# Optimization experiments

Hardware: AMD Instinct MI355X
Metric: run time of the kernel (lower is better)

Reference implementation:

```python
import jax, jax.numpy as jnp
import numpy as np

NT, NC = 100000, 25000
ETT, ECT = 800000, 400000
DIN_T, DIN_C = 64, 32
H, C = 4, 32
HID = H * C  # 128
SLOPE = 0.2  # GATConv LeakyReLU negative slope


def setup_inputs() -> dict:
    key = jax.random.key(0)
    ks = jax.random.split(key, 24)
    def p(i, shape, s=0.05):
        return jax.random.normal(ks[i], shape, dtype=jnp.float32) * s
    return {
        'x_target': jax.random.normal(ks[0], (NT, DIN_T), dtype=jnp.float32),
        'x_context': jax.random.normal(ks[1], (NC, DIN_C), dtype=jnp.float32),
        'edge_tt': jax.random.randint(ks[2], (2, ETT), 0, NT),
        'edge_ct_src': jax.random.randint(ks[3], (ECT,), 0, NC),
        'edge_ct_dst': jax.random.randint(ks[4], (ECT,), 0, NT),
        'W_pre_t': p(5, (DIN_T, HID)), 'b_pre_t': jnp.zeros((HID,), jnp.float32),
        'W_pre_c': p(6, (DIN_C, HID)), 'b_pre_c': jnp.zeros((HID,), jnp.float32),
        'W_sd': p(7, (HID, HID)), 'att_src_sd': p(8, (H, C)), 'att_dst_sd': p(9, (H, C)), 'b_sd': jnp.zeros((HID,), jnp.float32),
        'W_ds': p(10, (HID, HID)), 'att_src_ds': p(11, (H, C)), 'att_dst_ds': p(12, (H, C)), 'b_ds': jnp.zeros((HID,), jnp.float32),
        'W_ct_src': p(13, (HID, HID)), 'W_ct_dst': p(14, (HID, HID)), 'att_src_ct': p(15, (H, C)), 'att_dst_ct': p(16, (H, C)), 'b_ct': jnp.zeros((HID,), jnp.float32),
        'W_out': p(17, (HID, HID)), 'b_out': jnp.zeros((HID,), jnp.float32),
    }


def _gat(h_src, h_dst, att_s, att_d, src, dst, n_dst, bias):
    # h_src: [N_src,H,C] transformed src feats; h_dst: [N_dst,H,C]
    a_s = jnp.einsum('nhc,hc->nh', h_src, att_s)  # [N_src,H]
    a_d = jnp.einsum('nhc,hc->nh', h_dst, att_d)  # [N_dst,H]
    e = a_s[src] + a_d[dst]                        # [E,H]
    e = jnp.where(e > 0, e, SLOPE * e)             # LeakyReLU(0.2)
    m = jax.ops.segment_max(e, dst, num_segments=n_dst)  # stable softmax per dst
    ex = jnp.exp(e - m[dst])
    den = jax.ops.segment_sum(ex, dst, num_segments=n_dst)
    alpha = ex / den[dst]                          # [E,H]
    msg = h_src[src] * alpha[:, :, None]           # [E,H,C]
    out = jax.ops.segment_sum(msg, dst, num_segments=n_dst)
    return out.reshape(n_dst, H * C) + bias


def reference(x_target, x_context, edge_tt, edge_ct_src, edge_ct_dst,
              W_pre_t, b_pre_t, W_pre_c, b_pre_c,
              W_sd, att_src_sd, att_dst_sd, b_sd,
              W_ds, att_src_ds, att_dst_ds, b_ds,
              W_ct_src, W_ct_dst, att_src_ct, att_dst_ct, b_ct,
              W_out, b_out):
    # HeteroDictLinear pretransform + relu
    h_t = jax.nn.relu(x_target @ W_pre_t + b_pre_t)   # [NT,128]
    h_c = jax.nn.relu(x_context @ W_pre_c + b_pre_c)  # [NC,128]
    res = h_t
    # DirGATConv on (target,to,target): forward + reversed, each w/ self-loops
    loops = jnp.arange(NT)
    src_f = jnp.concatenate([edge_tt[0], loops]); dst_f = jnp.concatenate([edge_tt[1], loops])
    src_r = jnp.concatenate([edge_tt[1], loops]); dst_r = jnp.concatenate([edge_tt[0], loops])
    hs = (h_t @ W_sd).reshape(NT, H, C)
    out_sd = _gat(hs, hs, att_src_sd, att_dst_sd, src_f, dst_f, NT, b_sd)
    hd = (h_t @ W_ds).reshape(NT, H, C)
    out_ds = _gat(hd, hd, att_src_ds, att_dst_ds, src_r, dst_r, NT, b_ds)
    out_tt = 0.5 * out_sd + 0.5 * out_ds  # (1-alpha), alpha with alpha=0.5
    # bipartite GATConv on (context,to,target), no self loops
    hcs = (h_c @ W_ct_src).reshape(NC, H, C)
    htd = (h_t @ W_ct_dst).reshape(NT, H, C)
    out_ct = _gat(hcs, htd, att_src_ct, att_dst_ct, edge_ct_src, edge_ct_dst, NT, b_ct)
    # HeteroConv aggr='mean' over the two edge types hitting 'target'
    x = 0.5 * (out_tt + out_ct)
    x = jax.nn.relu(x + res)  # skip connection + relu
    return x @ W_out + b_out
```

## Files before the change

kernel.cpp:

```cpp
#include <hip/hip_runtime.h>
#include <cstdint>
#include <cstddef>

typedef unsigned short u16;
typedef unsigned int u32;

#define NT 100000
#define NC 25000
#define ETT 800000
#define ECT 400000
#define SLOPE 0.2f
#define OFFS (NT + 4)

#define NBK 782
#define NBLK 256
#define CHT ((ETT + NBLK - 1) / NBLK)
#define CHC ((ECT + NBLK - 1) / NBLK)
#define TOTC (3 * NBK * NBLK)
#define NSB ((TOTC + 2047) / 2048)

typedef __attribute__((ext_vector_type(8))) short bf16x8;
typedef __attribute__((ext_vector_type(4))) float f32x4;

__device__ __forceinline__ u16 f2bf(float f) {
  u32 u = __float_as_uint(f);
  u32 r = (u >> 16) & 1u;
  return (u16)((u + 0x7fffu + r) >> 16);
}
__device__ __forceinline__ float lof(u32 p) { return __uint_as_float(p << 16); }
__device__ __forceinline__ float hif(u32 p) { return __uint_as_float(p & 0xffff0000u); }

__global__ __launch_bounds__(256) void pre_t_kernel(const float* __restrict__ in,
    const float* __restrict__ W, const float* __restrict__ bias,
    const float* __restrict__ fold_cd, u16* __restrict__ h_t,
    float* __restrict__ aD, int N)
{
  __shared__ float s_in[32][33];
  __shared__ float s_W[32][128];
  __shared__ float s_fold[512];
  const int t = threadIdx.x;
  s_fold[t] = fold_cd[t];
  s_fold[t + 256] = fold_cd[t + 256];
  const int row0 = blockIdx.x * 32;
  const int rl = t >> 3, cg = t & 7;
  const int gr = row0 + rl;
  float acc[4][4];
  for (int g = 0; g < 4; ++g)
    for (int j = 0; j < 4; ++j)
      acc[g][j] = bias[g * 32 + cg * 4 + j];
  for (int kc = 0; kc < 64; kc += 32) {
    {
      float4 f = make_float4(0.f, 0.f, 0.f, 0.f);
      if (gr < N) f = *(const float4*)(in + (size_t)gr * 64 + kc + cg * 4);
      s_in[rl][cg * 4 + 0] = f.x; s_in[rl][cg * 4 + 1] = f.y;
      s_in[rl][cg * 4 + 2] = f.z; s_in[rl][cg * 4 + 3] = f.w;
    }
    for (int j = 0; j < 4; ++j) {
      const int idx = t + j * 256;
      const int k = idx >> 5, c4 = (idx & 31) * 4;
      *(float4*)&s_W[k][c4] = *(const float4*)(W + (size_t)(kc + k) * 128 + c4);
    }
    __syncthreads();
#pragma unroll 8
    for (int k = 0; k < 32; ++k) {
      const float a = s_in[rl][k];
      for (int g = 0; g < 4; ++g) {
        const float4 w = *(const float4*)&s_W[k][g * 32 + cg * 4];
        acc[g][0] = fmaf(a, w.x, acc[g][0]);
        acc[g][1] = fmaf(a, w.y, acc[g][1]);
        acc[g][2] = fmaf(a, w.z, acc[g][2]);
        acc[g][3] = fmaf(a, w.w, acc[g][3]);
      }
    }
    __syncthreads();
  }
  if (gr < N) {
    float p0 = 0.f, p1 = 0.f, p2 = 0.f, p3 = 0.f;
    for (int g = 0; g < 4; ++g) {
      for (int j = 0; j < 4; ++j) acc[g][j] = fmaxf(acc[g][j], 0.f);
      uint2 pk;
      pk.x = (u32)f2bf(acc[g][0]) | ((u32)f2bf(acc[g][1]) << 16);
      pk.y = (u32)f2bf(acc[g][2]) | ((u32)f2bf(acc[g][3]) << 16);
      *(uint2*)(h_t + (size_t)gr * 128 + g * 32 + cg * 4) = pk;
      for (int j = 0; j < 4; ++j) {
        const int col = g * 32 + cg * 4 + j;
        const float4 f4 = *(const float4*)&s_fold[col * 4];
        const float a = acc[g][j];
        p0 = fmaf(a, f4.x, p0); p1 = fmaf(a, f4.y, p1);
        p2 = fmaf(a, f4.z, p2); p3 = fmaf(a, f4.w, p3);
      }
    }
    for (int m = 1; m < 8; m <<= 1) {
      p0 += __shfl_xor(p0, m); p1 += __shfl_xor(p1, m);
      p2 += __shfl_xor(p2, m); p3 += __shfl_xor(p3, m);
    }
    if (cg == 0) *(float4*)(aD + (size_t)gr * 4) = make_float4(p0, p1, p2, p3);
  }
}

__global__ __launch_bounds__(256) void prep_kernel(
    const float* __restrict__ Wsd, const float* __restrict__ AsSd, const float* __restrict__ AdSd,
    const float* __restrict__ Wds, const float* __restrict__ AsDs, const float* __restrict__ AdDs,
    const float* __restrict__ Wout, u16* __restrict__ bf_sd, u16* __restrict__ bf_ds,
    u16* __restrict__ bf_out,
    const float* __restrict__ Wcd, const float* __restrict__ attD,
    const float* __restrict__ bsd, const float* __restrict__ bds, const float* __restrict__ bct,
    float* __restrict__ fold_cd, float* __restrict__ cbias)
{
  const int b = blockIdx.x;
  const int tid = threadIdx.x;
  if (b == 3) {
    if (tid < 128) {
      for (int h = 0; h < 4; ++h) {
        float s = 0.f;
        for (int c = 0; c < 32; ++c)
          s = fmaf(Wcd[tid * 128 + h * 32 + c], attD[h * 32 + c], s);
        fold_cd[tid * 4 + h] = s;
      }
      cbias[tid] = 0.25f * bsd[tid] + 0.25f * bds[tid] + 0.5f * bct[tid];
    }
    return;
  }
  __shared__ float fS[512], fD[512];
  const float* W = (b == 0) ? Wsd : (b == 1) ? Wds : Wout;
  const float* As = (b == 0) ? AsSd : AsDs;
  const float* Ad = (b == 0) ? AdSd : AdDs;
  u16* out = (b == 0) ? bf_sd : (b == 1) ? bf_ds : bf_out;
  const int tiles = (b == 2) ? 8 : 9;
  if (b < 2) {
    if (tid < 128) {
      for (int h = 0; h < 4; ++h) {
        float s1 = 0.f, s2 = 0.f;
        for (int c = 0; c < 32; ++c) {
          const float wv = W[tid * 128 + h * 32 + c];
          s1 = fmaf(wv, As[h * 32 + c], s1);
          s2 = fmaf(wv, Ad[h * 32 + c], s2);
        }
        fS[tid * 4 + h] = s1; fD[tid * 4 + h] = s2;
      }
    }
    __syncthreads();
  }
  const int total = tiles * 4 * 64 * 8;
  for (int i = tid; i < total; i += 256) {
    const int j = i & 7, lane = (i >> 3) & 63, ks = (i >> 9) & 3, t = i >> 11;
    const int k = ks * 32 + (lane >> 4) * 8 + j;
    const int n = t * 16 + (lane & 15);
    float v;
    if (n < 128) v = W[k * 128 + n];
    else if (n < 132) v = fS[k * 4 + (n - 128)];
    else if (n < 136) v = fD[k * 4 + (n - 132)];
    else v = 0.f;
    out[i] = f2bf(v);
  }
}

__global__ __launch_bounds__(256) void mfma_logits2_kernel(
    const short* __restrict__ A, const short* __restrict__ Bsd, const short* __restrict__ Bds,
    u16* __restrict__ hs, float* __restrict__ aSsd, float* __restrict__ aDsd,
    u16* __restrict__ hd, float* __restrict__ aSds, float* __restrict__ aDds, int M)
{
  __shared__ __align__(16) float lds[4][16][148];
  const int wv = threadIdx.x >> 6, lane = threadIdx.x & 63;
  const int quad = lane >> 4, l16 = lane & 15;
  const int row0 = blockIdx.x * 64 + wv * 16;
  const int arow = min(row0 + l16, M - 1);
  const short* ap = A + (size_t)arow * 128 + quad * 8;
  bf16x8 af[4];
  for (int ks = 0; ks < 4; ++ks) af[ks] = *(const bf16x8*)(ap + ks * 32);
  const int row = row0 + l16;
  const int idx = lane & 7, rr = lane >> 3;
  for (int pass = 0; pass < 2; ++pass) {
    const short* B = pass ? Bds : Bsd;
    u16* outb = pass ? hd : hs;
    float* aS = pass ? aSds : aSsd;
    float* aD = pass ? aDds : aDsd;
    f32x4 acc[9];
    for (int t = 0; t < 9; ++t) acc[t] = (f32x4){0.f, 0.f, 0.f, 0.f};
    for (int ks = 0; ks < 4; ++ks)
      for (int t = 0; t < 9; ++t) {
        const bf16x8 bf = *(const bf16x8*)(B + ((t * 4 + ks) * 64 + lane) * 8);
        acc[t] = __builtin_amdgcn_mfma_f32_16x16x32_bf16(af[ks], bf, acc[t], 0, 0, 0);
      }
    for (int t = 0; t < 9; ++t)
      for (int r = 0; r < 4; ++r)
        lds[wv][quad * 4 + r][t * 16 + l16] = acc[t][r];
    __syncthreads();
    if (row < M) {
      for (int g = 0; g < 8; ++g) {
        const f32x4 v = *(const f32x4*)&lds[wv][l16][g * 16 + quad * 4];
        uint2 pk;
        pk.x = (u32)f2bf(v[0]) | ((u32)f2bf(v[1]) << 16);
        pk.y = (u32)f2bf(v[2]) | ((u32)f2bf(v[3]) << 16);
        *(uint2*)(outb + (size_t)row * 128 + g * 16 + quad * 4) = pk;
      }
    }
    for (int p = 0; p < 2; ++p) {
      const int lr = p * 8 + rr;
      const int n = row0 + lr;
      if (n < M) {
        const float v = lds[wv][lr][128 + idx];
        if (idx < 4) aS[(size_t)n * 4 + idx] = v;
        else aD[(size_t)n * 4 + idx - 4] = v;
      }
    }
    __syncthreads();
  }
}

__global__ __launch_bounds__(256) void mfma_out_kernel(
    const short* __restrict__ A, const short* __restrict__ B,
    const float* __restrict__ bias, float* __restrict__ out, int M)
{
  __shared__ __align__(16) float lds[4][16][132];
  const int wv = threadIdx.x >> 6, lane = threadIdx.x & 63;
  const int quad = lane >> 4, l16 = lane & 15;
  const int row0 = blockIdx.x * 64 + wv * 16;
  const int arow = min(row0 + l16, M - 1);
  const short* ap = A + (size_t)arow * 128 + quad * 8;
  bf16x8 af[4];
  for (int ks = 0; ks < 4; ++ks) af[ks] = *(const bf16x8*)(ap + ks * 32);
  f32x4 acc[8];
  for (int t = 0; t < 8; ++t) acc[t] = (f32x4){0.f, 0.f, 0.f, 0.f};
  for (int ks = 0; ks < 4; ++ks)
    for (int t = 0; t < 8; ++t) {
      const bf16x8 bf = *(const bf16x8*)(B + ((t * 4 + ks) * 64 + lane) * 8);
      acc[t] = __builtin_amdgcn_mfma_f32_16x16x32_bf16(af[ks], bf, acc[t], 0, 0, 0);
    }
  for (int t = 0; t < 8; ++t)
    for (int r = 0; r < 4; ++r)
      lds[wv][quad * 4 + r][t * 16 + l16] = acc[t][r];
  __syncthreads();
  const int row = row0 + l16;
  if (row < M) {
    for (int g = 0; g < 8; ++g) {
      const int col = g * 16 + quad * 4;
      f32x4 v = *(const f32x4*)&lds[wv][l16][col];
      const f32x4 b4 = *(const f32x4*)(bias + col);
      v = v + b4;
      *(f32x4*)(out + (size_t)row * 128 + col) = v;
    }
  }
}

__global__ __launch_bounds__(256) void ctx_kernel(const float* __restrict__ x_c,
    const float* __restrict__ Wpc, const float* __restrict__ bpc,
    const float* __restrict__ Wcs, const float* __restrict__ attS,
    u16* __restrict__ hc_bf, float* __restrict__ aS, int N)
{
  __shared__ float s_in[32][33];
  __shared__ float s_W[32][128];
  __shared__ float s_h[32][132];
  const int t = threadIdx.x;
  const int row0 = blockIdx.x * 32;
  const int rl = t >> 3, cg = t & 7;
  const int gr = row0 + rl;
  {
    float4 f = make_float4(0.f, 0.f, 0.f, 0.f);
    if (gr < N) f = *(const float4*)(x_c + (size_t)gr * 32 + cg * 4);
    s_in[rl][cg * 4 + 0] = f.x; s_in[rl][cg * 4 + 1] = f.y;
    s_in[rl][cg * 4 + 2] = f.z; s_in[rl][cg * 4 + 3] = f.w;
  }
  for (int j = 0; j < 4; ++j) {
    const int idx = t + j * 256;
    const int k = idx >> 5, c4 = (idx & 31) * 4;
    *(float4*)&s_W[k][c4] = *(const float4*)(Wpc + (size_t)k * 128 + c4);
  }
  __syncthreads();
  float acc[4][4];
  for (int g = 0; g < 4; ++g)
    for (int j = 0; j < 4; ++j) acc[g][j] = bpc[g * 32 + cg * 4 + j];
#pragma unroll 8
  for (int k = 0; k < 32; ++k) {
    const float a = s_in[rl][k];
    for (int g = 0; g < 4; ++g) {
      const float4 w = *(const float4*)&s_W[k][g * 32 + cg * 4];
      acc[g][0] = fmaf(a, w.x, acc[g][0]);
      acc[g][1] = fmaf(a, w.y, acc[g][1]);
      acc[g][2] = fmaf(a, w.z, acc[g][2]);
      acc[g][3] = fmaf(a, w.w, acc[g][3]);
    }
  }
  for (int g = 0; g < 4; ++g)
    *(float4*)&s_h[rl][g * 32 + cg * 4] =
        make_float4(fmaxf(acc[g][0], 0.f), fmaxf(acc[g][1], 0.f),
                    fmaxf(acc[g][2], 0.f), fmaxf(acc[g][3], 0.f));
  __syncthreads();
  float acc2[4][4];
  for (int g = 0; g < 4; ++g)
    for (int j = 0; j < 4; ++j) acc2[g][j] = 0.f;
  for (int kc = 0; kc < 128; kc += 32) {
    for (int j = 0; j < 4; ++j) {
      const int idx = t + j * 256;
      const int k = idx >> 5, c4 = (idx & 31) * 4;
      *(float4*)&s_W[k][c4] = *(const float4*)(Wcs + (size_t)(kc + k) * 128 + c4);
    }
    __syncthreads();
#pragma unroll 8
    for (int k = 0; k < 32; ++k) {
      const float a = s_h[rl][kc + k];
      for (int g = 0; g < 4; ++g) {
        const float4 w = *(const float4*)&s_W[k][g * 32 + cg * 4];
        acc2[g][0] = fmaf(a, w.x, acc2[g][0]);
        acc2[g][1] = fmaf(a, w.y, acc2[g][1]);
        acc2[g][2] = fmaf(a, w.z, acc2[g][2]);
        acc2[g][3] = fmaf(a, w.w, acc2[g][3]);
      }
    }
    __syncthreads();
  }
  if (gr < N) {
    float pS[4];
    for (int g = 0; g < 4; ++g) {
      uint2 pk;
      pk.x = (u32)f2bf(acc2[g][0]) | ((u32)f2bf(acc2[g][1]) << 16);
      pk.y = (u32)f2bf(acc2[g][2]) | ((u32)f2bf(acc2[g][3]) << 16);
      *(uint2*)(hc_bf + (size_t)gr * 128 + g * 32 + cg * 4) = pk;
      const float4 as4 = *(const float4*)(attS + g * 32 + cg * 4);
      pS[g] = acc2[g][0] * as4.x + acc2[g][1] * as4.y + acc2[g][2] * as4.z + acc2[g][3] * as4.w;
    }
    for (int m = 1; m < 8; m <<= 1)
      for (int g = 0; g < 4; ++g) pS[g] += __shfl_xor(pS[g], m);
    if (cg == 0)
      *(float4*)(aS + (size_t)gr * 4) = make_float4(pS[0], pS[1], pS[2], pS[3]);
  }
}

__global__ __launch_bounds__(256) void hist_blk_kernel(const int* __restrict__ tt_src,
    const int* __restrict__ tt_dst, const int* __restrict__ ect_d, int* __restrict__ cntblk)
{
  __shared__ int h[3 * NBK];
  const int t = threadIdx.x, b = blockIdx.x;
  for (int i = t; i < 3 * NBK; i += 256) h[i] = 0;
  __syncthreads();
  const int lo = b * CHT, hi = min(lo + CHT, ETT);
  for (int i = lo + t; i < hi; i += 256) {
    atomicAdd(&h[tt_dst[i] >> 7], 1);
    atomicAdd(&h[NBK + (tt_src[i] >> 7)], 1);
  }
  const int lo2 = b * CHC, hi2 = min(lo2 + CHC, ECT);
  for (int i = lo2 + t; i < hi2; i += 256)
    atomicAdd(&h[2 * NBK + (ect_d[i] >> 7)], 1);
  __syncthreads();
  for (int i = t; i < 3 * NBK; i += 256)
    cntblk[(size_t)i * NBLK + b] = h[i];
}

__global__ __launch_bounds__(256) void scan2_blk_kernel(const int* __restrict__ in,
    int* __restrict__ out, int* __restrict__ bsum)
{
  const int t = threadIdx.x, b = blockIdx.x;
  const int idx = b * 2048 + t * 8;
  int v[8];
  int s = 0;
  if (idx < TOTC) {
    const int4 q0 = *(const int4*)(in + idx);
    const int4 q1 = *(const int4*)(in + idx + 4);
    int x;
    x = q0.x; v[0] = s; s += x;  x = q0.y; v[1] = s; s += x;
    x = q0.z; v[2] = s; s += x;  x = q0.w; v[3] = s; s += x;
    x = q1.x; v[4] = s; s += x;  x = q1.y; v[5] = s; s += x;
    x = q1.z; v[6] = s; s += x;  x = q1.w; v[7] = s; s += x;
  } else {
    for (int j = 0; j < 8; ++j) v[j] = 0;
  }
  __shared__ int sh[256];
  sh[t] = s;
  __syncthreads();
  for (int d = 1; d < 256; d <<= 1) {
    const int u = (t >= d) ? sh[t - d] : 0;
    __syncthreads();
    sh[t] += u;
    __syncthreads();
  }
  const int excl = (t == 0) ? 0 : sh[t - 1];
  if (idx < TOTC) {
    int4 q0, q1;
    q0.x = excl + v[0]; q0.y = excl + v[1]; q0.z = excl + v[2]; q0.w = excl + v[3];
    q1.x = excl + v[4]; q1.y = excl + v[5]; q1.z = excl + v[6]; q1.w = excl + v[7];
    *(int4*)(out + idx) = q0;
    *(int4*)(out + idx + 4) = q1;
  }
  if (t == 255) bsum[b] = sh[255];
}

__global__ __launch_bounds__(512) void scan2_top_kernel(const int* __restrict__ bsum,
    int* __restrict__ bpre)
{
  __shared__ int sh[512];
  const int t = threadIdx.x;
  const int orig = (t < NSB) ? bsum[t] : 0;
  sh[t] = orig;
  __syncthreads();
  for (int d = 1; d < 512; d <<= 1) {
    const int v = (t >= d) ? sh[t - d] : 0;
    __syncthreads();
    sh[t] += v;
    __syncthreads();
  }
  if (t < NSB) bpre[t] = sh[t] - orig;
}

__global__ __launch_bounds__(256) void scan2_add_kernel(const int* __restrict__ bpre,
    int* __restrict__ out)
{
  const int t = threadIdx.x, b = blockIdx.x;
  const int bp = bpre[b];
  const int idx = b * 2048 + t * 8;
  if (idx < TOTC) {
    int4 q0 = *(const int4*)(out + idx);
    int4 q1 = *(const int4*)(out + idx + 4);
    q0.x += bp; q0.y += bp; q0.z += bp; q0.w += bp;
    q1.x += bp; q1.y += bp; q1.z += bp; q1.w += bp;
    *(int4*)(out + idx) = q0;
    *(int4*)(out + idx + 4) = q1;
  }
}

__global__ __launch_bounds__(256) void bin_kernel(const int* __restrict__ tt_src,
    const int* __restrict__ tt_dst, const int* __restrict__ ect_s, const int* __restrict__ ect_d,
    const int* __restrict__ scanned, u32* __restrict__ bin)
{
  __shared__ int cur[3 * NBK];
  const int t = threadIdx.x, b = blockIdx.x;
  for (int i = t; i < 3 * NBK; i += 256)
    cur[i] = scanned[(size_t)i * NBLK + b];
  __syncthreads();
  const int lo = b * CHT, hi = min(lo + CHT, ETT);
  for (int i = lo + t; i < hi; i += 256) {
    const int s = tt_src[i], d = tt_dst[i];
    int p = atomicAdd(&cur[d >> 7], 1);
    bin[p] = ((u32)(d & 127) << 17) | (u32)s;
    p = atomicAdd(&cur[NBK + (s >> 7)], 1);
    bin[p] = ((u32)(s & 127) << 17) | (u32)d;
  }
  const int lo2 = b * CHC, hi2 = min(lo2 + CHC, ECT);
  for (int i = lo2 + t; i < hi2; i += 256) {
    const int s = ect_s[i], d = ect_d[i];
    const int p = atomicAdd(&cur[2 * NBK + (d >> 7)], 1);
    bin[p] = ((u32)(d & 127) << 17) | (u32)s;
  }
}

__global__ __launch_bounds__(256) void bucket_fill_kernel(const int* __restrict__ scanned,
    const u32* __restrict__ bin, int* __restrict__ offs, int* __restrict__ big_el)
{
  const int rel = blockIdx.x / NBK;
  const int bucket = blockIdx.x - rel * NBK;
  const int t = threadIdx.x;
  __shared__ int s_cnt[128], s_exc[128], s_cur[128];
  if (t < 128) s_cnt[t] = 0;
  __syncthreads();
  const int base = scanned[(size_t)blockIdx.x * NBLK];
  const int nxt = (blockIdx.x == 3 * NBK - 1) ? (2 * ETT + ECT)
                                              : scanned[((size_t)blockIdx.x + 1) * NBLK];
  const int size = nxt - base;
  for (int i = t; i < size; i += 256)
    atomicAdd(&s_cnt[bin[base + i] >> 17], 1);
  __syncthreads();
  if (t < 128) s_exc[t] = s_cnt[t];
  __syncthreads();
  for (int d = 1; d < 128; d <<= 1) {
    int v = 0;
    if (t < 128 && t >= d) v = s_exc[t - d];
    __syncthreads();
    if (t < 128) s_exc[t] += v;
    __syncthreads();
  }
  const int relbase = rel * ETT;
  const int obase = base - relbase;
  int* off_rel = offs + (size_t)rel * OFFS;
  const int node0 = bucket * 128;
  if (t < 128) {
    const int excl = s_exc[t] - s_cnt[t];
    s_cur[t] = obase + excl;
    if (node0 + t < NT) off_rel[node0 + t] = obase + excl;
  }
  if (t == 0 && bucket == NBK - 1) off_rel[NT] = obase + size;
  __syncthreads();
  int* el_rel = big_el + relbase;
  for (int i = t; i < size; i += 256) {
    const u32 e = bin[base + i];
    const int pos = atomicAdd(&s_cur[e >> 17], 1);
    el_rel[pos] = (int)(e & 0x1FFFFu);
  }
}

__device__ __forceinline__ void gat_pipe16(const int* __restrict__ off,
    const int* __restrict__ el, const float* __restrict__ aS, const float* __restrict__ aD,
    const u16* __restrict__ hb, int d, int h, int cb, int self_loop, float w,
    float* __restrict__ acc)
{
  const float ad = aD[(size_t)d * 4 + h];
  const int beg = off[d];
  const int m = off[d + 1] - beg;
  const int cnt = m + self_loop;
  if (cnt <= 0) return;
  float den = 0.f;
  float a0 = 0.f, a1 = 0.f, a2 = 0.f, a3 = 0.f, a4 = 0.f, a5 = 0.f, a6 = 0.f, a7 = 0.f;
  int sB = (1 < m) ? el[beg + 1] : d;
  {
    const int sA0 = (0 < m) ? el[beg] : d;
    float eA = aS[(size_t)sA0 * 4 + h];
    uint4 pA = *(const uint4*)(hb + (size_t)sA0 * 128 + cb);
    for (int k = 0; k < cnt; ++k) {
      const int sC = (k + 2 < m) ? el[beg + k + 2] : d;
      const float eB = aS[(size_t)sB * 4 + h];
      const uint4 pB = *(const uint4*)(hb + (size_t)sB * 128 + cb);
      float ea = eA + ad;
      ea = ea > 0.f ? ea : SLOPE * ea;
      const float ex = __expf(ea);
      den += ex;
      a0 = fmaf(ex, lof(pA.x), a0); a1 = fmaf(ex, hif(pA.x), a1);
      a2 = fmaf(ex, lof(pA.y), a2); a3 = fmaf(ex, hif(pA.y), a3);
      a4 = fmaf(ex, lof(pA.z), a4); a5 = fmaf(ex, hif(pA.z), a5);
      a6 = fmaf(ex, lof(pA.w), a6); a7 = fmaf(ex, hif(pA.w), a7);
      eA = eB; pA = pB; sB = sC;
    }
  }
  const float s = w / den;
  acc[0] = fmaf(a0, s, acc[0]); acc[1] = fmaf(a1, s, acc[1]);
  acc[2] = fmaf(a2, s, acc[2]); acc[3] = fmaf(a3, s, acc[3]);
  acc[4] = fmaf(a4, s, acc[4]); acc[5] = fmaf(a5, s, acc[5]);
  acc[6] = fmaf(a6, s, acc[6]); acc[7] = fmaf(a7, s, acc[7]);
}

__global__ __launch_bounds__(256) void gather_all_kernel(
    const int* __restrict__ off_f, const int* __restrict__ el_f,
    const float* __restrict__ aS_sd, const float* __restrict__ aD_sd, const u16* __restrict__ hs,
    const int* __restrict__ off_r, const int* __restrict__ el_r,
    const float* __restrict__ aS_ds, const float* __restrict__ aD_ds, const u16* __restrict__ hd,
    const int* __restrict__ off_c, const int* __restrict__ el_c,
    const float* __restrict__ aS_ct, const float* __restrict__ aD_ct, const u16* __restrict__ hc,
    const u16* __restrict__ skip, const float* __restrict__ cbias, u16* __restrict__ x)
{
  const int d = blockIdx.x * 16 + (threadIdx.x >> 4);
  if (d >= NT) return;
  const int lg = threadIdx.x & 15;
  const int h = lg >> 2;
  const int cb = lg * 8;
  float acc[8];
  for (int i = 0; i < 8; ++i) acc[i] = 0.f;
  gat_pipe16(off_f, el_f, aS_sd, aD_sd, hs, d, h, cb, 1, 0.25f, acc);
  gat_pipe16(off_r, el_r, aS_ds, aD_ds, hd, d, h, cb, 1, 0.25f, acc);
  gat_pipe16(off_c, el_c, aS_ct, aD_ct, hc, d, h, cb, 0, 0.5f, acc);
  const uint4 sk = *(const uint4*)(skip + (size_t)d * 128 + cb);
  const float4 cb0 = *(const float4*)(cbias + cb);
  const float4 cb1 = *(const float4*)(cbias + cb + 4);
  const float o0 = fmaxf(acc[0] + cb0.x + lof(sk.x), 0.f);
  const float o1 = fmaxf(acc[1] + cb0.y + hif(sk.x), 0.f);
  const float o2 = fmaxf(acc[2] + cb0.z + lof(sk.y), 0.f);
  const float o3 = fmaxf(acc[3] + cb0.w + hif(sk.y), 0.f);
  const float o4 = fmaxf(acc[4] + cb1.x + lof(sk.z), 0.f);
  const float o5 = fmaxf(acc[5] + cb1.y + hif(sk.z), 0.f);
  const float o6 = fmaxf(acc[6] + cb1.z + lof(sk.w), 0.f);
  const float o7 = fmaxf(acc[7] + cb1.w + hif(sk.w), 0.f);
  uint4 r;
  r.x = (u32)f2bf(o0) | ((u32)f2bf(o1) << 16);
  r.y = (u32)f2bf(o2) | ((u32)f2bf(o3) << 16);
  r.z = (u32)f2bf(o4) | ((u32)f2bf(o5) << 16);
  r.w = (u32)f2bf(o6) | ((u32)f2bf(o7) << 16);
  *(uint4*)(x + (size_t)d * 128 + cb) = r;
}

extern "C" void kernel_launch(void* const* d_in, const int* in_sizes, int n_in,
                              void* d_out, int out_size, void* d_ws, size_t ws_size,
                              hipStream_t stream)
{
  const float* x_t   = (const float*)d_in[0];
  const float* x_c   = (const float*)d_in[1];
  const int*   e_tt  = (const int*)d_in[2];
  const int*   ect_s = (const int*)d_in[3];
  const int*   ect_d = (const int*)d_in[4];
  const float* Wpt = (const float*)d_in[5];   const float* bpt = (const float*)d_in[6];
  const float* Wpc = (const float*)d_in[7];   const float* bpc = (const float*)d_in[8];
  const float* Wsd = (const float*)d_in[9];   const float* As_sd = (const float*)d_in[10];
  const float* Ad_sd = (const float*)d_in[11]; const float* bsd = (const float*)d_in[12];
  const float* Wds = (const float*)d_in[13];  const float* As_ds = (const float*)d_in[14];
  const float* Ad_ds = (const float*)d_in[15]; const float* bds = (const float*)d_in[16];
  const float* Wcs = (const float*)d_in[17];  const float* Wcd = (const float*)d_in[18];
  const float* As_ct = (const float*)d_in[19]; const float* Ad_ct = (const float*)d_in[20];
  const float* bct = (const float*)d_in[21];
  const float* Wout = (const float*)d_in[22]; const float* bout = (const float*)d_in[23];

  char* p = (char*)d_ws;
  size_t off = 0;
  auto alloc = [&](size_t bytes) { char* r = p + off; off += (bytes + 255) & ~(size_t)255; return r; };
  u16* ht_bf   = (u16*)alloc((size_t)NT * 128 * 2);
  u16* hs_bf   = (u16*)alloc((size_t)NT * 128 * 2);
  u16* hd_bf   = (u16*)alloc((size_t)NT * 128 * 2);
  u16* hc_bf   = (u16*)alloc((size_t)NC * 128 * 2);
  u16* x_bf    = (u16*)alloc((size_t)NT * 128 * 2);
  float* aS_sd = (float*)alloc((size_t)NT * 4 * 4);
  float* aD_sd = (float*)alloc((size_t)NT * 4 * 4);
  float* aS_ds = (float*)alloc((size_t)NT * 4 * 4);
  float* aD_ds = (float*)alloc((size_t)NT * 4 * 4);
  float* aS_ct = (float*)alloc((size_t)NC * 4 * 4);
  float* aD_ct = (float*)alloc((size_t)NT * 4 * 4);
  int* cntblk  = (int*)alloc((size_t)TOTC * 4);
  int* scanned = (int*)alloc((size_t)TOTC * 4);
  u32* bin     = (u32*)alloc((size_t)(2 * ETT + ECT) * 4);
  int* big_el  = (int*)alloc((size_t)(2 * ETT + ECT) * 4);
  int* offs    = (int*)alloc((size_t)3 * OFFS * 4);
  int* bsum    = (int*)alloc((size_t)NSB * 4);
  int* bpre    = (int*)alloc((size_t)NSB * 4);
  float* fold_cd = (float*)alloc(512 * 4);
  float* cbias   = (float*)alloc(128 * 4);
  u16* bfrag_sd  = (u16*)alloc((size_t)9 * 4 * 64 * 8 * 2);
  u16* bfrag_ds  = (u16*)alloc((size_t)9 * 4 * 64 * 8 * 2);
  u16* bfrag_out = (u16*)alloc((size_t)8 * 4 * 64 * 8 * 2);

  int* off_f = offs;
  int* off_r = offs + OFFS;
  int* off_c = offs + 2 * OFFS;
  int* el_f = big_el;
  int* el_r = big_el + ETT;
  int* el_c = big_el + 2 * ETT;

  const int* tt_src = e_tt;
  const int* tt_dst = e_tt + ETT;

  const int gT = (NT + 31) / 32;
  const int gC = (NC + 31) / 32;
  const int gM = (NT + 63) / 64;

  hist_blk_kernel<<<NBLK, 256, 0, stream>>>(tt_src, tt_dst, ect_d, cntblk);
  scan2_blk_kernel<<<NSB, 256, 0, stream>>>(cntblk, scanned, bsum);
  scan2_top_kernel<<<1, 512, 0, stream>>>(bsum, bpre);
  scan2_add_kernel<<<NSB, 256, 0, stream>>>(bpre, scanned);
  bin_kernel<<<NBLK, 256, 0, stream>>>(tt_src, tt_dst, ect_s, ect_d, scanned, bin);
  bucket_fill_kernel<<<3 * NBK, 256, 0, stream>>>(scanned, bin, offs, big_el);

  prep_kernel<<<4, 256, 0, stream>>>(Wsd, As_sd, Ad_sd, Wds, As_ds, Ad_ds, Wout,
                                     bfrag_sd, bfrag_ds, bfrag_out,
                                     Wcd, Ad_ct, bsd, bds, bct, fold_cd, cbias);

  pre_t_kernel<<<gT, 256, 0, stream>>>(x_t, Wpt, bpt, fold_cd, ht_bf, aD_ct, NT);
  mfma_logits2_kernel<<<gM, 256, 0, stream>>>((const short*)ht_bf,
      (const short*)bfrag_sd, (const short*)bfrag_ds,
      hs_bf, aS_sd, aD_sd, hd_bf, aS_ds, aD_ds, NT);
  ctx_kernel<<<gC, 256, 0, stream>>>(x_c, Wpc, bpc, Wcs, As_ct, hc_bf, aS_ct, NC);

  gather_all_kernel<<<(NT + 15) / 16, 256, 0, stream>>>(
      off_f, el_f, aS_sd, aD_sd, hs_bf,
      off_r, el_r, aS_ds, aD_ds, hd_bf,
      off_c, el_c, aS_ct, aD_ct, hc_bf,
      ht_bf, cbias, x_bf);

  mfma_out_kernel<<<gM, 256, 0, stream>>>((const short*)x_bf, (const short*)bfrag_out,
                                          bout, (float*)d_out, NT);
}
```

Baseline: 441.8 us.

## Merge prep, pre_t and ctx kernels; fold scan-add into consumers; use exp2

```diff
diff --git a/kernel.cpp b/kernel.cpp
--- a/kernel.cpp
+++ b/kernel.cpp
@@ -10,6 +10,7 @@
 #define ETT 800000
 #define ECT 400000
 #define SLOPE 0.2f
+#define LOG2E 1.4426950408889634f
 #define OFFS (NT + 4)
 
 #define NBK 782
@@ -30,128 +31,212 @@
 __device__ __forceinline__ float lof(u32 p) { return __uint_as_float(p << 16); }
 __device__ __forceinline__ float hif(u32 p) { return __uint_as_float(p & 0xffff0000u); }
 
-__global__ __launch_bounds__(256) void pre_t_kernel(const float* __restrict__ in,
-    const float* __restrict__ W, const float* __restrict__ bias,
-    const float* __restrict__ fold_cd, u16* __restrict__ h_t,
-    float* __restrict__ aD, int N)
-{
-  __shared__ float s_in[32][33];
-  __shared__ float s_W[32][128];
-  __shared__ float s_fold[512];
+#define GT_BLK ((NT + 31) / 32)
+#define GC_BLK ((NC + 31) / 32)
+
+__global__ __launch_bounds__(256) void transform_kernel(
+    const float* __restrict__ Wsd, const float* __restrict__ AsSd, const float* __restrict__ AdSd,
+    const float* __restrict__ Wds, const float* __restrict__ AsDs, const float* __restrict__ AdDs,
+    const float* __restrict__ Wout,
+    u16* __restrict__ bf_sd, u16* __restrict__ bf_ds, u16* __restrict__ bf_out,
+    const float* __restrict__ Wcd, const float* __restrict__ attD,
+    const float* __restrict__ bsd, const float* __restrict__ bds, const float* __restrict__ bct,
+    float* __restrict__ cbias,
+    const float* __restrict__ x_t, const float* __restrict__ Wpt, const float* __restrict__ bpt,
+    u16* __restrict__ h_t, float* __restrict__ aD,
+    const float* __restrict__ x_c, const float* __restrict__ Wpc, const float* __restrict__ bpc,
+    const float* __restrict__ Wcs, const float* __restrict__ attS,
+    u16* __restrict__ hc_bf, float* __restrict__ aS_c)
+{
+  __shared__ float s_a[32][33];
+  __shared__ float s_b[32][128];
+  __shared__ float s_c[32][132];
+  const int b = blockIdx.x;
   const int t = threadIdx.x;
-  s_fold[t] = fold_cd[t];
-  s_fold[t + 256] = fold_cd[t + 256];
-  const int row0 = blockIdx.x * 32;
-  const int rl = t >> 3, cg = t & 7;
-  const int gr = row0 + rl;
-  float acc[4][4];
-  for (int g = 0; g < 4; ++g)
-    for (int j = 0; j < 4; ++j)
-      acc[g][j] = bias[g * 32 + cg * 4 + j];
-  for (int kc = 0; kc < 64; kc += 32) {
+
+  if (b < 4) {
+    if (b == 3) {
+      if (t < 128) cbias[t] = 0.25f * bsd[t] + 0.25f * bds[t] + 0.5f * bct[t];
+      return;
+    }
+    float* fS = &s_c[0][0];
+    float* fD = fS + 512;
+    const float* W = (b == 0) ? Wsd : (b == 1) ? Wds : Wout;
+    const float* As = (b == 0) ? AsSd : AsDs;
+    const float* Ad = (b == 0) ? AdSd : AdDs;
+    u16* out = (b == 0) ? bf_sd : (b == 1) ? bf_ds : bf_out;
+    const int tiles = (b == 2) ? 8 : 9;
+    if (b < 2) {
+      if (t < 128) {
+        for (int h = 0; h < 4; ++h) {
+          float s1 = 0.f, s2 = 0.f;
+          for (int c = 0; c < 32; ++c) {
+            const float wv = W[t * 128 + h * 32 + c];
+            s1 = fmaf(wv, As[h * 32 + c], s1);
+            s2 = fmaf(wv, Ad[h * 32 + c], s2);
+          }
+          fS[t * 4 + h] = s1 * LOG2E; fD[t * 4 + h] = s2 * LOG2E;
+        }
+      }
+      __syncthreads();
+    }
+    const int total = tiles * 4 * 64 * 8;
+    for (int i = t; i < total; i += 256) {
+      const int j = i & 7, lane = (i >> 3) & 63, ks = (i >> 9) & 3, ti = i >> 11;
+      const int k = ks * 32 + (lane >> 4) * 8 + j;
+      const int n = ti * 16 + (lane & 15);
+      float v;
+      if (n < 128) v = W[k * 128 + n];
+      else if (n < 132) v = fS[k * 4 + (n - 128)];
+      else if (n < 136) v = fD[k * 4 + (n - 132)];
+      else v = 0.f;
+      out[i] = f2bf(v);
+    }
+    return;
+  }
+
+  if (b < 4 + GT_BLK) {
+    float* s_fold = &s_c[0][0];
+    if (t < 128) {
+      for (int h = 0; h < 4; ++h) {
+        float s = 0.f;
+        for (int c = 0; c < 32; ++c)
+          s = fmaf(Wcd[t * 128 + h * 32 + c], attD[h * 32 + c], s);
+        s_fold[t * 4 + h] = s * LOG2E;
+      }
+    }
+    const int row0 = (b - 4) * 32;
+    const int rl = t >> 3, cg = t & 7;
+    const int gr = row0 + rl;
+    float acc[4][4];
+    for (int g = 0; g < 4; ++g)
+      for (int j = 0; j < 4; ++j)
+        acc[g][j] = bpt[g * 32 + cg * 4 + j];
+    for (int kc = 0; kc < 64; kc += 32) {
+      {
+        float4 f = make_float4(0.f, 0.f, 0.f, 0.f);
+        if (gr < NT) f = *(const float4*)(x_t + (size_t)gr * 64 + kc + cg * 4);
+        s_a[rl][cg * 4 + 0] = f.x; s_a[rl][cg * 4 + 1] = f.y;
+        s_a[rl][cg * 4 + 2] = f.z; s_a[rl][cg * 4 + 3] = f.w;
+      }
+      for (int j = 0; j < 4; ++j) {
+        const int idx = t + j * 256;
+        const int k = idx >> 5, c4 = (idx & 31) * 4;
+        *(float4*)&s_b[k][c4] = *(const float4*)(Wpt + (size_t)(kc + k) * 128 + c4);
+      }
+      __syncthreads();
+#pragma unroll 8
+      for (int k = 0; k < 32; ++k) {
+        const float a = s_a[rl][k];
+        for (int g = 0; g < 4; ++g) {
+          const float4 w = *(const float4*)&s_b[k][g * 32 + cg * 4];
+          acc[g][0] = fmaf(a, w.x, acc[g][0]);
+          acc[g][1] = fmaf(a, w.y, acc[g][1]);
+          acc[g][2] = fmaf(a, w.z, acc[g][2]);
+          acc[g][3] = fmaf(a, w.w, acc[g][3]);
+        }
+      }
+      __syncthreads();
+    }
+    if (gr < NT) {
+      float p0 = 0.f, p1 = 0.f, p2 = 0.f, p3 = 0.f;
+      for (int g = 0; g < 4; ++g) {
+        for (int j = 0; j < 4; ++j) acc[g][j] = fmaxf(acc[g][j], 0.f);
+        uint2 pk;
+        pk.x = (u32)f2bf(acc[g][0]) | ((u32)f2bf(acc[g][1]) << 16);
+        pk.y = (u32)f2bf(acc[g][2]) | ((u32)f2bf(acc[g][3]) << 16);
+        *(uint2*)(h_t + (size_t)gr * 128 + g * 32 + cg * 4) = pk;
+        for (int j = 0; j < 4; ++j) {
+          const int col = g * 32 + cg * 4 + j;
+          const float4 f4 = *(const float4*)&s_fold[col * 4];
+          const float a = acc[g][j];
+          p0 = fmaf(a, f4.x, p0); p1 = fmaf(a, f4.y, p1);
+          p2 = fmaf(a, f4.z, p2); p3 = fmaf(a, f4.w, p3);
+        }
+      }
+      for (int m = 1; m < 8; m <<= 1) {
+        p0 += __shfl_xor(p0, m); p1 += __shfl_xor(p1, m);
+        p2 += __shfl_xor(p2, m); p3 += __shfl_xor(p3, m);
+      }
+      if (cg == 0) *(float4*)(aD + (size_t)gr * 4) = make_float4(p0, p1, p2, p3);
+    }
+    return;
+  }
+
+  {
+    const int row0 = (b - 4 - GT_BLK) * 32;
+    const int rl = t >> 3, cg = t & 7;
+    const int gr = row0 + rl;
     {
       float4 f = make_float4(0.f, 0.f, 0.f, 0.f);
-      if (gr < N) f = *(const float4*)(in + (size_t)gr * 64 + kc + cg * 4);
-      s_in[rl][cg * 4 + 0] = f.x; s_in[rl][cg * 4 + 1] = f.y;
-      s_in[rl][cg * 4 + 2] = f.z; s_in[rl][cg * 4 + 3] = f.w;
+      if (gr < NC) f = *(const float4*)(x_c + (size_t)gr * 32 + cg * 4);
+      s_a[rl][cg * 4 + 0] = f.x; s_a[rl][cg * 4 + 1] = f.y;
+      s_a[rl][cg * 4 + 2] = f.z; s_a[rl][cg * 4 + 3] = f.w;
     }
     for (int j = 0; j < 4; ++j) {
       const int idx = t + j * 256;
       const int k = idx >> 5, c4 = (idx & 31) * 4;
-      *(float4*)&s_W[k][c4] = *(const float4*)(W + (size_t)(kc + k) * 128 + c4);
-    }
-    __syncthreads();
+      *(float4*)&s_b[k][c4] = *(const float4*)(Wpc + (size_t)k * 128 + c4);
+    }
+    __syncthreads();
+    float acc[4][4];
+    for (int g = 0; g < 4; ++g)
+      for (int j = 0; j < 4; ++j) acc[g][j] = bpc[g * 32 + cg * 4 + j];
 #pragma unroll 8
     for (int k = 0; k < 32; ++k) {
-      const float a = s_in[rl][k];
+      const float a = s_a[rl][k];
       for (int g = 0; g < 4; ++g) {
-        const float4 w = *(const float4*)&s_W[k][g * 32 + cg * 4];
+        const float4 w = *(const float4*)&s_b[k][g * 32 + cg * 4];
         acc[g][0] = fmaf(a, w.x, acc[g][0]);
         acc[g][1] = fmaf(a, w.y, acc[g][1]);
         acc[g][2] = fmaf(a, w.z, acc[g][2]);
         acc[g][3] = fmaf(a, w.w, acc[g][3]);
       }
     }
-    __syncthreads();
-  }
-  if (gr < N) {
-    float p0 = 0.f, p1 = 0.f, p2 = 0.f, p3 = 0.f;
-    for (int g = 0; g < 4; ++g) {
-      for (int j = 0; j < 4; ++j) acc[g][j] = fmaxf(acc[g][j], 0.f);
-      uint2 pk;
-      pk.x = (u32)f2bf(acc[g][0]) | ((u32)f2bf(acc[g][1]) << 16);
-      pk.y = (u32)f2bf(acc[g][2]) | ((u32)f2bf(acc[g][3]) << 16);
-      *(uint2*)(h_t + (size_t)gr * 128 + g * 32 + cg * 4) = pk;
+    for (int g = 0; g < 4; ++g)
+      *(float4*)&s_c[rl][g * 32 + cg * 4] =
+          make_float4(fmaxf(acc[g][0], 0.f), fmaxf(acc[g][1], 0.f),
+                      fmaxf(acc[g][2], 0.f), fmaxf(acc[g][3], 0.f));
+    __syncthreads();
+    float acc2[4][4];
+    for (int g = 0; g < 4; ++g)
+      for (int j = 0; j < 4; ++j) acc2[g][j] = 0.f;
+    for (int kc = 0; kc < 128; kc += 32) {
       for (int j = 0; j < 4; ++j) {
-        const int col = g * 32 + cg * 4 + j;
-        const float4 f4 = *(const float4*)&s_fold[col * 4];
-        const float a = acc[g][j];
-        p0 = fmaf(a, f4.x, p0); p1 = fmaf(a, f4.y, p1);
-        p2 = fmaf(a, f4.z, p2); p3 = fmaf(a, f4.w, p3);
-      }
-    }
-    for (int m = 1; m < 8; m <<= 1) {
-      p0 += __shfl_xor(p0, m); p1 += __shfl_xor(p1, m);
-      p2 += __shfl_xor(p2, m); p3 += __shfl_xor(p3, m);
-    }
-    if (cg == 0) *(float4*)(aD + (size_t)gr * 4) = make_float4(p0, p1, p2, p3);
-  }
-}
-
-__global__ __launch_bounds__(256) void prep_kernel(
-    const float* __restrict__ Wsd, const float* __restrict__ AsSd, const float* __restrict__ AdSd,
-    const float* __restrict__ Wds, const float* __restrict__ AsDs, const float* __restrict__ AdDs,
-    const float* __restrict__ Wout, u16* __restrict__ bf_sd, u16* __restrict__ bf_ds,
-    u16* __restrict__ bf_out,
-    const float* __restrict__ Wcd, const float* __restrict__ attD,
-    const float* __restrict__ bsd, const float* __restrict__ bds, const float* __restrict__ bct,
-    float* __restrict__ fold_cd, float* __restrict__ cbias)
-{
-  const int b = blockIdx.x;
-  const int tid = threadIdx.x;
-  if (b == 3) {
-    if (tid < 128) {
-      for (int h = 0; h < 4; ++h) {
-        float s = 0.f;
-        for (int c = 0; c < 32; ++c)
-          s = fmaf(Wcd[tid * 128 + h * 32 + c], attD[h * 32 + c], s);
-        fold_cd[tid * 4 + h] = s;
-      }
-      cbias[tid] = 0.25f * bsd[tid] + 0.25f * bds[tid] + 0.5f * bct[tid];
-    }
-    return;
-  }
-  __shared__ float fS[512], fD[512];
-  const float* W = (b == 0) ? Wsd : (b == 1) ? Wds : Wout;
-  const float* As = (b == 0) ? AsSd : AsDs;
-  const float* Ad = (b == 0) ? AdSd : AdDs;
-  u16* out = (b == 0) ? bf_sd : (b == 1) ? bf_ds : bf_out;
-  const int tiles = (b == 2) ? 8 : 9;
-  if (b < 2) {
-    if (tid < 128) {
-      for (int h = 0; h < 4; ++h) {
-        float s1 = 0.f, s2 = 0.f;
-        for (int c = 0; c < 32; ++c) {
-          const float wv = W[tid * 128 + h * 32 + c];
-          s1 = fmaf(wv, As[h * 32 + c], s1);
-          s2 = fmaf(wv, Ad[h * 32 + c], s2);
+        const int idx = t + j * 256;
+        const int k = idx >> 5, c4 = (idx & 31) * 4;
+        *(float4*)&s_b[k][c4] = *(const float4*)(Wcs + (size_t)(kc + k) * 128 + c4);
+      }
+      __syncthreads();
+#pragma unroll 8
+      for (int k = 0; k < 32; ++k) {
+        const float a = s_c[rl][kc + k];
+        for (int g = 0; g < 4; ++g) {
+          const float4 w = *(const float4*)&s_b[k][g * 32 + cg * 4];
+          acc2[g][0] = fmaf(a, w.x, acc2[g][0]);
+          acc2[g][1] = fmaf(a, w.y, acc2[g][1]);
+          acc2[g][2] = fmaf(a, w.z, acc2[g][2]);
+          acc2[g][3] = fmaf(a, w.w, acc2[g][3]);
         }
-        fS[tid * 4 + h] = s1; fD[tid * 4 + h] = s2;
-      }
-    }
-    __syncthreads();
-  }
-  const int total = tiles * 4 * 64 * 8;
-  for (int i = tid; i < total; i += 256) {
-    const int j = i & 7, lane = (i >> 3) & 63, ks = (i >> 9) & 3, t = i >> 11;
-    const int k = ks * 32 + (lane >> 4) * 8 + j;
-    const int n = t * 16 + (lane & 15);
-    float v;
-    if (n < 128) v = W[k * 128 + n];
-    else if (n < 132) v = fS[k * 4 + (n - 128)];
-    else if (n < 136) v = fD[k * 4 + (n - 132)];
-    else v = 0.f;
-    out[i] = f2bf(v);
+      }
+      __syncthreads();
+    }
+    if (gr < NC) {
+      float pS[4];
+      for (int g = 0; g < 4; ++g) {
+        uint2 pk;
+        pk.x = (u32)f2bf(acc2[g][0]) | ((u32)f2bf(acc2[g][1]) << 16);
+        pk.y = (u32)f2bf(acc2[g][2]) | ((u32)f2bf(acc2[g][3]) << 16);
+        *(uint2*)(hc_bf + (size_t)gr * 128 + g * 32 + cg * 4) = pk;
+        const float4 as4 = *(const float4*)(attS + g * 32 + cg * 4);
+        pS[g] = acc2[g][0] * as4.x + acc2[g][1] * as4.y + acc2[g][2] * as4.z + acc2[g][3] * as4.w;
+      }
+      for (int m = 1; m < 8; m <<= 1)
+        for (int g = 0; g < 4; ++g) pS[g] += __shfl_xor(pS[g], m);
+      if (cg == 0)
+        *(float4*)(aS_c + (size_t)gr * 4) =
+            make_float4(pS[0] * LOG2E, pS[1] * LOG2E, pS[2] * LOG2E, pS[3] * LOG2E);
+    }
   }
 }
 
@@ -243,89 +328,6 @@
   }
 }
 
-__global__ __launch_bounds__(256) void ctx_kernel(const float* __restrict__ x_c,
-    const float* __restrict__ Wpc, const float* __restrict__ bpc,
-    const float* __restrict__ Wcs, const float* __restrict__ attS,
-    u16* __restrict__ hc_bf, float* __restrict__ aS, int N)
-{
-  __shared__ float s_in[32][33];
-  __shared__ float s_W[32][128];
-  __shared__ float s_h[32][132];
-  const int t = threadIdx.x;
-  const int row0 = blockIdx.x * 32;
-  const int rl = t >> 3, cg = t & 7;
-  const int gr = row0 + rl;
-  {
-    float4 f = make_float4(0.f, 0.f, 0.f, 0.f);
-    if (gr < N) f = *(const float4*)(x_c + (size_t)gr * 32 + cg * 4);
-    s_in[rl][cg * 4 + 0] = f.x; s_in[rl][cg * 4 + 1] = f.y;
-    s_in[rl][cg * 4 + 2] = f.z; s_in[rl][cg * 4 + 3] = f.w;
-  }
-  for (int j = 0; j < 4; ++j) {
-    const int idx = t + j * 256;
-    const int k = idx >> 5, c4 = (idx & 31) * 4;
-    *(float4*)&s_W[k][c4] = *(const float4*)(Wpc + (size_t)k * 128 + c4);
-  }
-  __syncthreads();
-  float acc[4][4];
-  for (int g = 0; g < 4; ++g)
-    for (int j = 0; j < 4; ++j) acc[g][j] = bpc[g * 32 + cg * 4 + j];
-#pragma unroll 8
-  for (int k = 0; k < 32; ++k) {
-    const float a = s_in[rl][k];
-    for (int g = 0; g < 4; ++g) {
-      const float4 w = *(const float4*)&s_W[k][g * 32 + cg * 4];
-      acc[g][0] = fmaf(a, w.x, acc[g][0]);
-      acc[g][1] = fmaf(a, w.y, acc[g][1]);
-      acc[g][2] = fmaf(a, w.z, acc[g][2]);
-      acc[g][3] = fmaf(a, w.w, acc[g][3]);
-    }
-  }
-  for (int g = 0; g < 4; ++g)
-    *(float4*)&s_h[rl][g * 32 + cg * 4] =
-        make_float4(fmaxf(acc[g][0], 0.f), fmaxf(acc[g][1], 0.f),
-                    fmaxf(acc[g][2], 0.f), fmaxf(acc[g][3], 0.f));
-  __syncthreads();
-  float acc2[4][4];
-  for (int g = 0; g < 4; ++g)
-    for (int j = 0; j < 4; ++j) acc2[g][j] = 0.f;
-  for (int kc = 0; kc < 128; kc += 32) {
-    for (int j = 0; j < 4; ++j) {
-      const int idx = t + j * 256;
-      const int k = idx >> 5, c4 = (idx & 31) * 4;
-      *(float4*)&s_W[k][c4] = *(const float4*)(Wcs + (size_t)(kc + k) * 128 + c4);
-    }
-    __syncthreads();
-#pragma unroll 8
-    for (int k = 0; k < 32; ++k) {
-      const float a = s_h[rl][kc + k];
-      for (int g = 0; g < 4; ++g) {
-        const float4 w = *(const float4*)&s_W[k][g * 32 + cg * 4];
-        acc2[g][0] = fmaf(a, w.x, acc2[g][0]);
-        acc2[g][1] = fmaf(a, w.y, acc2[g][1]);
-        acc2[g][2] = fmaf(a, w.z, acc2[g][2]);
-        acc2[g][3] = fmaf(a, w.w, acc2[g][3]);
-      }
-    }
-    __syncthreads();
-  }
-  if (gr < N) {
-    float pS[4];
-    for (int g = 0; g < 4; ++g) {
-      uint2 pk;
-      pk.x = (u32)f2bf(acc2[g][0]) | ((u32)f2bf(acc2[g][1]) << 16);
-      pk.y = (u32)f2bf(acc2[g][2]) | ((u32)f2bf(acc2[g][3]) << 16);
-      *(uint2*)(hc_bf + (size_t)gr * 128 + g * 32 + cg * 4) = pk;
-      const float4 as4 = *(const float4*)(attS + g * 32 + cg * 4);
-      pS[g] = acc2[g][0] * as4.x + acc2[g][1] * as4.y + acc2[g][2] * as4.z + acc2[g][3] * as4.w;
-    }
-    for (int m = 1; m < 8; m <<= 1)
-      for (int g = 0; g < 4; ++g) pS[g] += __shfl_xor(pS[g], m);
-    if (cg == 0)
-      *(float4*)(aS + (size_t)gr * 4) = make_float4(pS[0], pS[1], pS[2], pS[3]);
-  }
-}
-
 __global__ __launch_bounds__(256) void hist_blk_kernel(const int* __restrict__ tt_src,
     const int* __restrict__ tt_dst, const int* __restrict__ ect_d, int* __restrict__ cntblk)
 {
@@ -401,30 +403,16 @@
   if (t < NSB) bpre[t] = sh[t] - orig;
 }
 
-__global__ __launch_bounds__(256) void scan2_add_kernel(const int* __restrict__ bpre,
-    int* __restrict__ out)
-{
-  const int t = threadIdx.x, b = blockIdx.x;
-  const int bp = bpre[b];
-  const int idx = b * 2048 + t * 8;
-  if (idx < TOTC) {
-    int4 q0 = *(const int4*)(out + idx);
-    int4 q1 = *(const int4*)(out + idx + 4);
-    q0.x += bp; q0.y += bp; q0.z += bp; q0.w += bp;
-    q1.x += bp; q1.y += bp; q1.z += bp; q1.w += bp;
-    *(int4*)(out + idx) = q0;
-    *(int4*)(out + idx + 4) = q1;
-  }
-}
-
 __global__ __launch_bounds__(256) void bin_kernel(const int* __restrict__ tt_src,
     const int* __restrict__ tt_dst, const int* __restrict__ ect_s, const int* __restrict__ ect_d,
-    const int* __restrict__ scanned, u32* __restrict__ bin)
+    const int* __restrict__ scanned, const int* __restrict__ bpre, u32* __restrict__ bin)
 {
   __shared__ int cur[3 * NBK];
   const int t = threadIdx.x, b = blockIdx.x;
-  for (int i = t; i < 3 * NBK; i += 256)
-    cur[i] = scanned[(size_t)i * NBLK + b];
+  for (int i = t; i < 3 * NBK; i += 256) {
+    const int idx = i * NBLK + b;
+    cur[i] = scanned[idx] + bpre[idx >> 11];
+  }
   __syncthreads();
   const int lo = b * CHT, hi = min(lo + CHT, ETT);
   for (int i = lo + t; i < hi; i += 256) {
@@ -443,7 +431,8 @@
 }
 
 __global__ __launch_bounds__(256) void bucket_fill_kernel(const int* __restrict__ scanned,
-    const u32* __restrict__ bin, int* __restrict__ offs, int* __restrict__ big_el)
+    const int* __restrict__ bpre, const u32* __restrict__ bin,
+    int* __restrict__ offs, int* __restrict__ big_el)
 {
   const int rel = blockIdx.x / NBK;
   const int bucket = blockIdx.x - rel * NBK;
@@ -451,9 +440,10 @@
   __shared__ int s_cnt[128], s_exc[128], s_cur[128];
   if (t < 128) s_cnt[t] = 0;
   __syncthreads();
-  const int base = scanned[(size_t)blockIdx.x * NBLK];
+  const int bi = blockIdx.x * NBLK;
+  const int base = scanned[bi] + bpre[bi >> 11];
   const int nxt = (blockIdx.x == 3 * NBK - 1) ? (2 * ETT + ECT)
-                                              : scanned[((size_t)blockIdx.x + 1) * NBLK];
+                                              : scanned[bi + NBLK] + bpre[(bi + NBLK) >> 11];
   const int size = nxt - base;
   for (int i = t; i < size; i += 256)
     atomicAdd(&s_cnt[bin[base + i] >> 17], 1);
@@ -509,7 +499,7 @@
       const uint4 pB = *(const uint4*)(hb + (size_t)sB * 128 + cb);
       float ea = eA + ad;
       ea = ea > 0.f ? ea : SLOPE * ea;
-      const float ex = __expf(ea);
+      const float ex = exp2f(ea);
       den += ex;
       a0 = fmaf(ex, lof(pA.x), a0); a1 = fmaf(ex, hif(pA.x), a1);
       a2 = fmaf(ex, lof(pA.y), a2); a3 = fmaf(ex, hif(pA.y), a3);
@@ -604,7 +594,6 @@
   int* offs    = (int*)alloc((size_t)3 * OFFS * 4);
   int* bsum    = (int*)alloc((size_t)NSB * 4);
   int* bpre    = (int*)alloc((size_t)NSB * 4);
-  float* fold_cd = (float*)alloc(512 * 4);
   float* cbias   = (float*)alloc(128 * 4);
   u16* bfrag_sd  = (u16*)alloc((size_t)9 * 4 * 64 * 8 * 2);
   u16* bfrag_ds  = (u16*)alloc((size_t)9 * 4 * 64 * 8 * 2);
@@ -620,26 +609,24 @@
   const int* tt_src = e_tt;
   const int* tt_dst = e_tt + ETT;
 
-  const int gT = (NT + 31) / 32;
-  const int gC = (NC + 31) / 32;
   const int gM = (NT + 63) / 64;
 
   hist_blk_kernel<<<NBLK, 256, 0, stream>>>(tt_src, tt_dst, ect_d, cntblk);
   scan2_blk_kernel<<<NSB, 256, 0, stream>>>(cntblk, scanned, bsum);
   scan2_top_kernel<<<1, 512, 0, stream>>>(bsum, bpre);
-  scan2_add_kernel<<<NSB, 256, 0, stream>>>(bpre, scanned);
-  bin_kernel<<<NBLK, 256, 0, stream>>>(tt_src, tt_dst, ect_s, ect_d, scanned, bin);
-  bucket_fill_kernel<<<3 * NBK, 256, 0, stream>>>(scanned, bin, offs, big_el);
-
-  prep_kernel<<<4, 256, 0, stream>>>(Wsd, As_sd, Ad_sd, Wds, As_ds, Ad_ds, Wout,
-                                     bfrag_sd, bfrag_ds, bfrag_out,
-                                     Wcd, Ad_ct, bsd, bds, bct, fold_cd, cbias);
-
-  pre_t_kernel<<<gT, 256, 0, stream>>>(x_t, Wpt, bpt, fold_cd, ht_bf, aD_ct, NT);
+  bin_kernel<<<NBLK, 256, 0, stream>>>(tt_src, tt_dst, ect_s, ect_d, scanned, bpre, bin);
+  bucket_fill_kernel<<<3 * NBK, 256, 0, stream>>>(scanned, bpre, bin, offs, big_el);
+
+  transform_kernel<<<4 + GT_BLK + GC_BLK, 256, 0, stream>>>(
+      Wsd, As_sd, Ad_sd, Wds, As_ds, Ad_ds, Wout,
+      bfrag_sd, bfrag_ds, bfrag_out,
+      Wcd, Ad_ct, bsd, bds, bct, cbias,
+      x_t, Wpt, bpt, ht_bf, aD_ct,
+      x_c, Wpc, bpc, Wcs, As_ct, hc_bf, aS_ct);
+
   mfma_logits2_kernel<<<gM, 256, 0, stream>>>((const short*)ht_bf,
       (const short*)bfrag_sd, (const short*)bfrag_ds,
       hs_bf, aS_sd, aD_sd, hd_bf, aS_ds, aD_ds, NT);
-  ctx_kernel<<<gC, 256, 0, stream>>>(x_c, Wpc, bpc, Wcs, As_ct, hc_bf, aS_ct, NC);
 
   gather_all_kernel<<<(NT + 15) / 16, 256, 0, stream>>>(
       off_f, el_f, aS_sd, aD_sd, hs_bf,
```

After: 428.4 us. 1.03x faster.
